# Kernel tuning notes

Measured on AMD Instinct MI355X. Metric: run time of the kernel, lower is better.

## Reference

```python
import jax, jax.numpy as jnp
import numpy as np
import math

H = 768
NH = 12
DK = H // NH
EPS = 1e-12

def gelu(x):
    return 0.5 * x * (1 + jnp.tanh(math.sqrt(2 / math.pi) * (x + 0.044715 * x ** 3)))

def layernorm(x, w, b):
    u = x.mean(-1, keepdims=True)
    s = ((x - u) ** 2).mean(-1, keepdims=True)
    return w * (x - u) / jnp.sqrt(s + EPS) + b

def setup_inputs() -> dict:
    key = jax.random.key(0)
    ks = jax.random.split(key, 12)
    B, S = 4, 2048
    std = 1.0 / math.sqrt(H)
    inp = {
        'x': jax.random.normal(ks[0], (B, S, H), jnp.float32),
        'mask': jax.random.randint(ks[1], (B, S), 0, 2, jnp.int32),
        'wq': jax.random.normal(ks[2], (H, H), jnp.float32) * std,
        'wk': jax.random.normal(ks[3], (H, H), jnp.float32) * std,
        'wv': jax.random.normal(ks[4], (H, H), jnp.float32) * std,
        'wo': jax.random.normal(ks[5], (H, H), jnp.float32) * std,
        'wo_b': jnp.zeros((H,), jnp.float32),
        'w1': jax.random.normal(ks[6], (H, 4 * H), jnp.float32) * std,
        'w1_b': jnp.zeros((4 * H,), jnp.float32),
        'w2': jax.random.normal(ks[7], (4 * H, H), jnp.float32) * (0.5 / math.sqrt(H)),
        'w2_b': jnp.zeros((H,), jnp.float32),
        'ln1_w': jnp.ones((H,), jnp.float32),
        'ln1_b': jnp.zeros((H,), jnp.float32),
        'ln2_w': jnp.ones((H,), jnp.float32),
        'ln2_b': jnp.zeros((H,), jnp.float32),
    }
    return inp

def reference(x, mask, wq, wk, wv, wo, wo_b, w1, w1_b, w2, w2_b, ln1_w, ln1_b, ln2_w, ln2_b):
    B, S, _ = x.shape
    # --- attention sublayer (pre-LN, residual) ---
    y = layernorm(x, ln1_w, ln1_b)
    q = (y @ wq).reshape(B, S, NH, DK).transpose(0, 2, 1, 3)
    k = (y @ wk).reshape(B, S, NH, DK).transpose(0, 2, 1, 3)
    v = (y @ wv).reshape(B, S, NH, DK).transpose(0, 2, 1, 3)
    scores = jnp.einsum('bhqd,bhkd->bhqk', q, k) / math.sqrt(DK)
    m2 = (mask[:, :, None] * mask[:, None, :])[:, None, :, :]  # [B,1,S,S]
    scores = jnp.where(m2 == 0, jnp.float32(-1e9), scores)
    p = jax.nn.softmax(scores, axis=-1)
    ctx = jnp.einsum('bhqk,bhkd->bhqd', p, v).transpose(0, 2, 1, 3).reshape(B, S, H)
    x = x + ctx @ wo + wo_b
    # --- FFN sublayer ---
    y2 = layernorm(x, ln2_w, ln2_b)
    x = x + gelu(y2 @ w1 + w1_b) @ w2 + w2_b
    return x
```

## Files before the change

### kernel.cpp

```cpp
#include <hip/hip_runtime.h>
#include <hip/hip_bf16.h>

#define HD   768
#define BSZ  4
#define SEQ  2048
#define NTOK (BSZ*SEQ)
#define NHD  12
#define DKD  64

typedef __bf16 bf16_t;
typedef __bf16 bf16x8 __attribute__((ext_vector_type(8)));
typedef __bf16 bf16x4 __attribute__((ext_vector_type(4)));
typedef float  f32x4  __attribute__((ext_vector_type(4)));

__device__ __forceinline__ void async16(const void* g, void* l) {
    __builtin_amdgcn_global_load_lds(
        (const __attribute__((address_space(1))) unsigned int*)g,
        (__attribute__((address_space(3))) unsigned int*)l, 16, 0, 0);
}

__global__ __launch_bounds__(256) void prep_kernel(
    const float* __restrict__ wq, const float* __restrict__ wk,
    const float* __restrict__ wv, const float* __restrict__ wo,
    const float* __restrict__ w1, const float* __restrict__ w2,
    const int* __restrict__ mask,
    bf16_t* __restrict__ wqkvT, bf16_t* __restrict__ woT,
    bf16_t* __restrict__ w1T, bf16_t* __restrict__ w2T,
    float* __restrict__ mb)
{
    const int bid = blockIdx.x, t = threadIdx.x;
    if (bid >= 6912) {
        const int i = (bid - 6912) * 256 + t;
        mb[i] = mask[i] ? 0.f : -1e9f;
        return;
    }
    const float* in; bf16_t* out; int K, N, ktile, ntile;
    if (bid < 2304) {
        const int wsel = bid / 576, tt = bid % 576;
        const float* srcs[4] = { wq, wk, wv, wo };
        bf16_t* dsts[4] = { wqkvT, wqkvT + 768*768, wqkvT + 2*768*768, woT };
        in = srcs[wsel]; out = dsts[wsel]; K = 768; N = 768;
        ktile = tt / 24; ntile = tt % 24;
    } else if (bid < 4608) {
        const int tt = bid - 2304;
        in = w1; out = w1T; K = 768; N = 3072;
        ktile = tt / 96; ntile = tt % 96;
    } else {
        const int tt = bid - 4608;
        in = w2; out = w2T; K = 3072; N = 768;
        ktile = tt / 24; ntile = tt % 24;
    }
    __shared__ float tile[32][33];
    const int k0 = ktile * 32, n0 = ntile * 32;
    const int r = t >> 5, c = t & 31;
#pragma unroll
    for (int j = 0; j < 4; j++)
        tile[r + 8*j][c] = in[(size_t)(k0 + r + 8*j) * N + n0 + c];
    __syncthreads();
#pragma unroll
    for (int j = 0; j < 4; j++)
        out[(size_t)(n0 + r + 8*j) * K + k0 + c] = (bf16_t)tile[c][r + 8*j];
}

__global__ __launch_bounds__(256) void ln_kernel(
    const float* __restrict__ x, const float* __restrict__ gw,
    const float* __restrict__ gb, bf16_t* __restrict__ y)
{
    const int row = blockIdx.x, t = threadIdx.x;
    const float* xr = x + (size_t)row * HD;
    float v0 = xr[t], v1 = xr[t + 256], v2 = xr[t + 512];
    float s1 = v0 + v1 + v2;
    float s2 = v0*v0 + v1*v1 + v2*v2;
#pragma unroll
    for (int m = 1; m < 64; m <<= 1) {
        s1 += __shfl_xor(s1, m);
        s2 += __shfl_xor(s2, m);
    }
    __shared__ float red[8];
    const int w = t >> 6, l = t & 63;
    if (l == 0) { red[w] = s1; red[4 + w] = s2; }
    __syncthreads();
    s1 = red[0] + red[1] + red[2] + red[3];
    s2 = red[4] + red[5] + red[6] + red[7];
    float mean = s1 * (1.f/HD);
    float var  = fmaxf(s2 * (1.f/HD) - mean*mean, 0.f);
    float rstd = rsqrtf(var + 1e-12f);
    bf16_t* yr = y + (size_t)row * HD;
    yr[t]       = (bf16_t)(gw[t]      * (v0 - mean) * rstd + gb[t]);
    yr[t + 256] = (bf16_t)(gw[t + 256]* (v1 - mean) * rstd + gb[t + 256]);
    yr[t + 512] = (bf16_t)(gw[t + 512]* (v2 - mean) * rstd + gb[t + 512]);
}

template<int EPI>
__global__ __launch_bounds__(256) void gemm_bt(
    const bf16_t* __restrict__ A, const bf16_t* __restrict__ BT,
    const float* __restrict__ bias, const float* __restrict__ resid,
    void* __restrict__ outv, int M, int N, int K, int ldo,
    bf16_t* __restrict__ vtout)
{
    __shared__ __align__(16) unsigned char lds[49152];
    const int t = threadIdx.x;
    const int w = t >> 6, l = t & 63;
    const int wr = w >> 1, wc = w & 1;
    const int lr = l & 15, lg = l >> 4;
    const int nwg = gridDim.x * gridDim.y;
    int flat = blockIdx.y * gridDim.x + blockIdx.x;
    flat = (flat & 7) * (nwg >> 3) + (flat >> 3);
    const int bx = flat % gridDim.x, by = flat / gridDim.x;
    const int m0 = by * 128, n0 = bx * 128;

    const bf16_t* a_src = A  + (size_t)(m0 + (t >> 2)) * K + (t & 3) * 8;
    const bf16_t* b_src = BT + (size_t)(n0 + (t >> 2)) * K + (t & 3) * 8;
    f32x4 acc[4][4] = {};

    auto stage = [&](int kt, int buf) {
        unsigned char* d = lds + buf * 16384 + t * 16;
        async16(a_src + kt,                 d);
        async16(a_src + (size_t)64*K + kt,  d + 4096);
        async16(b_src + kt,                 d + 8192);
        async16(b_src + (size_t)64*K + kt,  d + 12288);
    };

    const int nt = K >> 5;
    stage(0, 0);
    stage(32, 1);
    asm volatile("s_waitcnt vmcnt(4)" ::: "memory");
    __builtin_amdgcn_s_barrier();

    int cur = 0;
    for (int it = 0; it < nt; ++it) {
        const bool pre = (it + 2 < nt);
        if (pre) {
            int b2 = cur + 2; if (b2 >= 3) b2 -= 3;
            stage((it + 2) << 5, b2);
        }
        const unsigned char* bufp = lds + cur * 16384;
        bf16x8 af[4], bfr[4];
#pragma unroll
        for (int n = 0; n < 4; n++)
            bfr[n] = *(const bf16x8*)(bufp + 8192 + (wc*64 + n*16 + lr)*64 + lg*16);
#pragma unroll
        for (int m = 0; m < 4; m++)
            af[m] = *(const bf16x8*)(bufp + (wr*64 + m*16 + lr)*64 + lg*16);
        __builtin_amdgcn_s_setprio(1);
#pragma unroll
        for (int m = 0; m < 4; m++)
#pragma unroll
            for (int n = 0; n < 4; n++)
                acc[m][n] = __builtin_amdgcn_mfma_f32_16x16x32_bf16(af[m], bfr[n], acc[m][n], 0, 0, 0);
        __builtin_amdgcn_s_setprio(0);
        if (it + 1 < nt) {
            asm volatile("s_waitcnt lgkmcnt(0)" ::: "memory");
            if (pre) asm volatile("s_waitcnt vmcnt(4)" ::: "memory");
            else     asm volatile("s_waitcnt vmcnt(0)" ::: "memory");
            __builtin_amdgcn_s_barrier();
        }
        cur = (cur + 1 == 3) ? 0 : cur + 1;
    }

#pragma unroll
    for (int m = 0; m < 4; m++) {
#pragma unroll
        for (int n = 0; n < 4; n++) {
            const int gc  = n0 + wc*64 + n*16 + lr;
            const int gr0 = m0 + wr*64 + m*16 + lg*4;
            if constexpr (EPI == 3) {
                if (gc >= 1536) {
                    const int hh = (gc - 1536) >> 6, dd = (gc - 1536) & 63;
                    const int bb = gr0 >> 11, ss = gr0 & 2047;
                    bf16x4 ov;
#pragma unroll
                    for (int i = 0; i < 4; i++) ov[i] = (bf16_t)acc[m][n][i];
                    *(bf16x4*)(vtout + ((size_t)(bb*NHD + hh)*64 + dd)*SEQ + ss) = ov;
                    continue;
                }
            }
#pragma unroll
            for (int i = 0; i < 4; i++) {
                const int gr = gr0 + i;
                float v = acc[m][n][i];
                if constexpr (EPI == 0 || EPI == 3) {
                    ((bf16_t*)outv)[(size_t)gr * ldo + gc] = (bf16_t)v;
                } else if constexpr (EPI == 1) {
                    ((float*)outv)[(size_t)gr * ldo + gc] =
                        v + bias[gc] + resid[(size_t)gr * ldo + gc];
                } else {
                    v += bias[gc];
                    float u = 0.7978845608028654f * (v + 0.044715f * v * v * v);
                    float g = v / (1.f + __expf(-2.f * u));
                    ((bf16_t*)outv)[(size_t)gr * ldo + gc] = (bf16_t)g;
                }
            }
        }
    }
}

__global__ __launch_bounds__(256) void attn_kernel(
    const bf16_t* __restrict__ qkv, const bf16_t* __restrict__ vt,
    const int* __restrict__ mask, const float* __restrict__ mbias,
    bf16_t* __restrict__ ctx)
{
    __shared__ __align__(16) unsigned char lds[16384];
    const int t = threadIdx.x, w = t >> 6, l = t & 63;
    const int lr = l & 15, lg = l >> 4;
    int flat = blockIdx.y * 16 + blockIdx.x;
    flat = (flat & 7) * 96 + (flat >> 3);
    const int bh = flat >> 4, qt = flat & 15;
    const int b = bh / NHD, h = bh % NHD;
    const int q0 = qt * 128 + w * 32;
    const int swz = (lr & 7) << 4;

    bf16x8 qf[2][2];
#pragma unroll
    for (int r = 0; r < 2; r++)
#pragma unroll
        for (int ks = 0; ks < 2; ks++)
            qf[r][ks] = *(const bf16x8*)(qkv + (size_t)(b*SEQ + q0 + r*16 + lr)*2304
                                         + h*64 + ks*32 + lg*8);
    int mq[2];
#pragma unroll
    for (int r = 0; r < 2; r++)
        mq[r] = mask[b*SEQ + q0 + r*16 + lr];

    float mrow[2] = { -INFINITY, -INFINITY };
    float lsum[2] = { 0.f, 0.f };
    f32x4 accO[2][4] = {};

    const bf16_t* kbase = qkv + (size_t)(b*SEQ)*2304 + 768 + h*64 + lg*8;
    const bf16_t* vbase = vt + (size_t)bh*64*SEQ + lg*8;
    unsigned char* plds = lds + w*4096;

    for (int kt = 0; kt < SEQ; kt += 64) {
        bf16x8 kf[4][2];
#pragma unroll
        for (int n = 0; n < 4; n++)
#pragma unroll
            for (int ks = 0; ks < 2; ks++)
                kf[n][ks] = *(const bf16x8*)(kbase
                              + (size_t)(kt + n*16 + lr)*2304 + ks*32);
        f32x4 mb[4];
#pragma unroll
        for (int n = 0; n < 4; n++)
            mb[n] = *(const f32x4*)(mbias + (size_t)b*SEQ + kt + n*16 + lg*4);

        f32x4 accS[4][2] = {};
        __builtin_amdgcn_s_setprio(1);
#pragma unroll
        for (int n = 0; n < 4; n++)
#pragma unroll
            for (int r = 0; r < 2; r++)
#pragma unroll
                for (int ks = 0; ks < 2; ks++)
                    accS[n][r] = __builtin_amdgcn_mfma_f32_16x16x32_bf16(
                        kf[n][ks], qf[r][ks], accS[n][r], 0, 0, 0);
        __builtin_amdgcn_s_setprio(0);

        bf16x8 vf[4][2];
#pragma unroll
        for (int dn = 0; dn < 4; dn++)
#pragma unroll
            for (int ks = 0; ks < 2; ks++)
                vf[dn][ks] = *(const bf16x8*)(vbase
                               + (size_t)(dn*16 + lr)*SEQ + kt + ks*32);

#pragma unroll
        for (int r = 0; r < 2; r++) {
            f32x4 sl[4];
#pragma unroll
            for (int n = 0; n < 4; n++)
#pragma unroll
                for (int i = 0; i < 4; i++)
                    sl[n][i] = mq[r] ? (accS[n][r][i] * 0.125f + mb[n][i]) : -1e9f;
            float px = -INFINITY;
#pragma unroll
            for (int n = 0; n < 4; n++)
                px = fmaxf(px, fmaxf(fmaxf(sl[n][0], sl[n][1]),
                                     fmaxf(sl[n][2], sl[n][3])));
            px = fmaxf(px, __shfl_xor(px, 16));
            px = fmaxf(px, __shfl_xor(px, 32));
            const float mold = mrow[r];
            if (!__all(px <= mold + 8.f)) {
                const float mnew = fmaxf(mold, px);
                const float sc = __expf(mold - mnew);
                lsum[r] *= sc;
#pragma unroll
                for (int dn = 0; dn < 4; dn++) accO[r][dn] *= sc;
                mrow[r] = mnew;
            }
            const float m = mrow[r];
            float ps = 0.f;
#pragma unroll
            for (int n = 0; n < 4; n++) {
                bf16x4 pk;
#pragma unroll
                for (int i = 0; i < 4; i++) {
                    float pv = __expf(sl[n][i] - m);
                    ps += pv;
                    pk[i] = (bf16_t)pv;
                }
                *(bf16x4*)(plds + (r*16 + lr)*128 + ((n*32 + lg*8) ^ swz)) = pk;
            }
            ps += __shfl_xor(ps, 16);
            ps += __shfl_xor(ps, 32);
            lsum[r] += ps;
        }

        bf16x8 pf[2][2];
#pragma unroll
        for (int r = 0; r < 2; r++)
#pragma unroll
            for (int ks = 0; ks < 2; ks++)
                pf[r][ks] = *(const bf16x8*)(plds + (r*16 + lr)*128
                                             + ((ks*64 + lg*16) ^ swz));
        __builtin_amdgcn_s_setprio(1);
#pragma unroll
        for (int r = 0; r < 2; r++)
#pragma unroll
            for (int dn = 0; dn < 4; dn++)
#pragma unroll
                for (int ks = 0; ks < 2; ks++)
                    accO[r][dn] = __builtin_amdgcn_mfma_f32_16x16x32_bf16(
                        vf[dn][ks], pf[r][ks], accO[r][dn], 0, 0, 0);
        __builtin_amdgcn_s_setprio(0);
    }

#pragma unroll
    for (int r = 0; r < 2; r++) {
        const float inv = 1.f / lsum[r];
#pragma unroll
        for (int dn = 0; dn < 4; dn++) {
            bf16x4 ov;
#pragma unroll
            for (int i = 0; i < 4; i++)
                ov[i] = (bf16_t)(accO[r][dn][i] * inv);
            *(bf16x4*)(ctx + (size_t)(b*SEQ + q0 + r*16 + lr)*HD
                       + h*64 + dn*16 + lg*4) = ov;
        }
    }
}

extern "C" void kernel_launch(void* const* d_in, const int* in_sizes, int n_in,
                              void* d_out, int out_size, void* d_ws, size_t ws_size,
                              hipStream_t stream)
{
    const float* x     = (const float*)d_in[0];
    const int*   mask  = (const int*)  d_in[1];
    const float* wq    = (const float*)d_in[2];
    const float* wk    = (const float*)d_in[3];
    const float* wv    = (const float*)d_in[4];
    const float* wo    = (const float*)d_in[5];
    const float* wo_b  = (const float*)d_in[6];
    const float* w1    = (const float*)d_in[7];
    const float* w1_b  = (const float*)d_in[8];
    const float* w2    = (const float*)d_in[9];
    const float* w2_b  = (const float*)d_in[10];
    const float* ln1_w = (const float*)d_in[11];
    const float* ln1_b = (const float*)d_in[12];
    const float* ln2_w = (const float*)d_in[13];
    const float* ln2_b = (const float*)d_in[14];

    unsigned char* ws = (unsigned char*)d_ws;
    size_t o = 0;
    auto alloc = [&](size_t bytes) {
        size_t r = o; o += (bytes + 255) & ~(size_t)255; return r;
    };
    bf16_t* wqkvT = (bf16_t*)(ws + alloc((size_t)2304*768*2));
    bf16_t* woT   = (bf16_t*)(ws + alloc((size_t)768*768*2));
    bf16_t* w1T   = (bf16_t*)(ws + alloc((size_t)3072*768*2));
    bf16_t* w2T   = (bf16_t*)(ws + alloc((size_t)768*3072*2));
    bf16_t* y     = (bf16_t*)(ws + alloc((size_t)NTOK*HD*2));
    float*  x1    = (float*) (ws + alloc((size_t)NTOK*HD*4));
    bf16_t* ctx   = (bf16_t*)(ws + alloc((size_t)NTOK*HD*2));
    float*  mbias = (float*) (ws + alloc((size_t)NTOK*4));
    bf16_t* qkv   = (bf16_t*)(ws + alloc((size_t)NTOK*2304*2));
    bf16_t* vt    = (bf16_t*)(ws + alloc((size_t)48*64*SEQ*2));
    bf16_t* hbuf  = qkv;
    (void)in_sizes; (void)n_in; (void)out_size; (void)ws_size;

    prep_kernel<<<6944,256,0,stream>>>(wq, wk, wv, wo, w1, w2, mask,
                                       wqkvT, woT, w1T, w2T, mbias);
    ln_kernel<<<NTOK,256,0,stream>>>(x, ln1_w, ln1_b, y);
    gemm_bt<3><<<dim3(18,64),256,0,stream>>>(y, wqkvT, nullptr, nullptr, qkv,
                                             NTOK, 2304, 768, 2304, vt);
    attn_kernel<<<dim3(16,48),256,0,stream>>>(qkv, vt, mask, mbias, ctx);
    gemm_bt<1><<<dim3(6,64),256,0,stream>>>(ctx, woT, wo_b, x, x1,
                                            NTOK, 768, 768, 768, nullptr);
    ln_kernel<<<NTOK,256,0,stream>>>(x1, ln2_w, ln2_b, y);
    gemm_bt<2><<<dim3(24,64),256,0,stream>>>(y, w1T, w1_b, nullptr, hbuf,
                                             NTOK, 3072, 768, 3072, nullptr);
    gemm_bt<1><<<dim3(6,64),256,0,stream>>>(hbuf, w2T, w2_b, x1, d_out,
                                            NTOK, 768, 3072, 768, nullptr);
}
```

Baseline: 487.1 us.

## Stage K/V tiles in shared LDS with double-buffered async loads in attention

```diff
diff --git a/kernel.cpp b/kernel.cpp
--- a/kernel.cpp
+++ b/kernel.cpp
@@ -200,7 +200,7 @@
     const int* __restrict__ mask, const float* __restrict__ mbias,
     bf16_t* __restrict__ ctx)
 {
-    __shared__ __align__(16) unsigned char lds[16384];
+    __shared__ __align__(16) unsigned char lds[49152];
     const int t = threadIdx.x, w = t >> 6, l = t & 63;
     const int lr = l & 15, lg = l >> 4;
     int flat = blockIdx.y * 16 + blockIdx.x;
@@ -226,23 +226,39 @@
     float lsum[2] = { 0.f, 0.f };
     f32x4 accO[2][4] = {};
 
-    const bf16_t* kbase = qkv + (size_t)(b*SEQ)*2304 + 768 + h*64 + lg*8;
-    const bf16_t* vbase = vt + (size_t)bh*64*SEQ + lg*8;
-    unsigned char* plds = lds + w*4096;
-
+    auto stage_kv = [&](int kt, int buf) {
+        unsigned char* d = lds + buf * 16384;
+#pragma unroll
+        for (int i2 = 0; i2 < 2; i2++) {
+            const int c = i2*256 + t;
+            const int row = c >> 3;
+            const int scol = ((c & 7) ^ (row & 7)) * 8;
+            async16(qkv + (size_t)(b*SEQ + kt + row)*2304 + 768 + h*64 + scol,
+                    d + c*16);
+            async16(vt + ((size_t)bh*64 + row)*SEQ + kt + scol,
+                    d + 8192 + c*16);
+        }
+    };
+
+    stage_kv(0, 0);
+    __syncthreads();
+
+    int cur = 0;
     for (int kt = 0; kt < SEQ; kt += 64) {
-        bf16x8 kf[4][2];
-#pragma unroll
-        for (int n = 0; n < 4; n++)
-#pragma unroll
-            for (int ks = 0; ks < 2; ks++)
-                kf[n][ks] = *(const bf16x8*)(kbase
-                              + (size_t)(kt + n*16 + lr)*2304 + ks*32);
+        if (kt + 64 < SEQ) stage_kv(kt + 64, cur ^ 1);
         f32x4 mb[4];
 #pragma unroll
         for (int n = 0; n < 4; n++)
             mb[n] = *(const f32x4*)(mbias + (size_t)b*SEQ + kt + n*16 + lg*4);
-
+        const unsigned char* bufp = lds + cur * 16384;
+
+        bf16x8 kf[4][2];
+#pragma unroll
+        for (int n = 0; n < 4; n++)
+#pragma unroll
+            for (int ks = 0; ks < 2; ks++)
+                kf[n][ks] = *(const bf16x8*)(bufp + (n*16 + lr)*128
+                                             + ((ks*64 + lg*16) ^ swz));
         f32x4 accS[4][2] = {};
         __builtin_amdgcn_s_setprio(1);
 #pragma unroll
@@ -254,14 +270,6 @@
                     accS[n][r] = __builtin_amdgcn_mfma_f32_16x16x32_bf16(
                         kf[n][ks], qf[r][ks], accS[n][r], 0, 0, 0);
         __builtin_amdgcn_s_setprio(0);
-
-        bf16x8 vf[4][2];
-#pragma unroll
-        for (int dn = 0; dn < 4; dn++)
-#pragma unroll
-            for (int ks = 0; ks < 2; ks++)
-                vf[dn][ks] = *(const bf16x8*)(vbase
-                               + (size_t)(dn*16 + lr)*SEQ + kt + ks*32);
 
 #pragma unroll
         for (int r = 0; r < 2; r++) {
@@ -298,19 +306,26 @@
                     ps += pv;
                     pk[i] = (bf16_t)pv;
                 }
-                *(bf16x4*)(plds + (r*16 + lr)*128 + ((n*32 + lg*8) ^ swz)) = pk;
+                *(bf16x4*)(lds + 32768 + w*4096 + (r*16 + lr)*128
+                           + ((n*32 + lg*8) ^ swz)) = pk;
             }
             ps += __shfl_xor(ps, 16);
             ps += __shfl_xor(ps, 32);
             lsum[r] += ps;
         }
 
-        bf16x8 pf[2][2];
+        bf16x8 vf[4][2], pf[2][2];
+#pragma unroll
+        for (int dn = 0; dn < 4; dn++)
+#pragma unroll
+            for (int ks = 0; ks < 2; ks++)
+                vf[dn][ks] = *(const bf16x8*)(bufp + 8192 + (dn*16 + lr)*128
+                                              + ((ks*64 + lg*16) ^ swz));
 #pragma unroll
         for (int r = 0; r < 2; r++)
 #pragma unroll
             for (int ks = 0; ks < 2; ks++)
-                pf[r][ks] = *(const bf16x8*)(plds + (r*16 + lr)*128
+                pf[r][ks] = *(const bf16x8*)(lds + 32768 + w*4096 + (r*16 + lr)*128
                                              + ((ks*64 + lg*16) ^ swz));
         __builtin_amdgcn_s_setprio(1);
 #pragma unroll
@@ -322,6 +337,9 @@
                     accO[r][dn] = __builtin_amdgcn_mfma_f32_16x16x32_bf16(
                         vf[dn][ks], pf[r][ks], accO[r][dn], 0, 0, 0);
         __builtin_amdgcn_s_setprio(0);
+
+        __syncthreads();
+        cur ^= 1;
     }
 
 #pragma unroll
```

New measurement: 413.7 us. -15.1%, faster.
